# Performance work log

Hardware: AMD Instinct MI355X
Metric: run time of the kernel (lower is better)

Reference implementation:

```python
import jax, jax.numpy as jnp
import numpy as np

N, C, H, K = 32768, 128, 4, 16
D = C // H  # head_dim = 32


def setup_inputs() -> dict:
    key = jax.random.key(0)
    ks = jax.random.split(key, 8)
    feats = jax.random.normal(ks[0], (N, C), dtype=jnp.float32)
    coords = jax.random.normal(ks[1], (N, 3), dtype=jnp.float32)
    knn_idx = jax.random.randint(ks[2], (N, K), 0, N, dtype=jnp.int64)
    s = 0.02
    Wq = jax.random.normal(ks[3], (C, C), dtype=jnp.float32) * s
    Wk = jax.random.normal(ks[4], (C, C), dtype=jnp.float32) * s
    Wv = jax.random.normal(ks[5], (C, C), dtype=jnp.float32) * s
    Wo = jax.random.normal(ks[6], (C, C), dtype=jnp.float32) * s
    bo = jnp.zeros((C,), dtype=jnp.float32)
    return {"feats": feats, "coords": coords, "knn_idx": knn_idx,
            "Wq": Wq, "Wk": Wk, "Wv": Wv, "Wo": Wo, "bo": bo}


def reference(feats, coords, knn_idx, Wq, Wk, Wv, Wo, bo):
    # coords only feeds the kNN search (precomputed as knn_idx)
    n, c = feats.shape
    q = (feats @ Wq.T).reshape(n, H, D)          # [N,H,D]
    k = (feats @ Wk.T).reshape(n, H, D)          # [N,H,D]
    v = (feats @ Wv.T).reshape(n, H, D)          # [N,H,D]
    kn = k[knn_idx]                               # gather -> [N,K,H,D]
    vn = v[knn_idx]                               # gather -> [N,K,H,D]
    scores = jnp.einsum('nhd,nkhd->nhk', q, kn) / jnp.sqrt(jnp.float32(D))
    w = jax.nn.softmax(scores, axis=-1)           # softmax over K neighbors
    out = jnp.einsum('nhk,nkhd->nhd', w, vn).reshape(n, c)
    return out @ Wo.T + bo
```

## Files before the change

kernel.cpp:

```cpp
#include <hip/hip_runtime.h>

#define NPTS 32768
#define C 128
#define KNBR 16

typedef __attribute__((ext_vector_type(8))) short short8;
typedef __attribute__((ext_vector_type(4))) float floatx4;
typedef __attribute__((ext_vector_type(4))) int intx4;

__device__ __forceinline__ ushort f2b(float f) {
    union { float f; uint u; } x; x.f = f;
    uint r = (x.u + 0x7fffu + ((x.u >> 16) & 1u)) >> 16;
    return (ushort)r;
}
__device__ __forceinline__ ushort f2h(float f) {
    union { _Float16 h; ushort u; } x; x.h = (_Float16)f; return x.u;
}
__device__ __forceinline__ float h2f(ushort u) {
    union { ushort u; _Float16 h; } x; x.u = u; return (float)x.h;
}

__device__ __forceinline__ int col_of(int w, int b) {
    return 64 * (w >> 4) + 32 * ((w >> 3) & 1) + 16 * (b & 1) + 2 * (w & 7) + (b >> 1);
}

__device__ __forceinline__ void stage128_b(const ushort* __restrict__ gsrc, ushort* lds, int tid)
{
#pragma unroll
    for (int it = 0; it < 8; ++it) {
        const int f = it * 256 + tid;
        const int row = f >> 4, slot = f & 15;
        intx4 v = *(const intx4*)(gsrc + (size_t)f * 8);
        *(intx4*)(lds + ((row * 16 + (slot ^ (row & 7))) * 8)) = v;
    }
}
__device__ __forceinline__ void stage128_f(const float* __restrict__ gsrc, ushort* lds, int tid)
{
#pragma unroll
    for (int it = 0; it < 8; ++it) {
        const int f = it * 256 + tid;
        const int row = f >> 4, slot = f & 15;
        const float* s = gsrc + (size_t)f * 8;
        float4 v0 = *(const float4*)s;
        float4 v1 = *(const float4*)(s + 4);
        intx4 o;
        o.x = (int)((uint)f2b(v0.x) | ((uint)f2b(v0.y) << 16));
        o.y = (int)((uint)f2b(v0.z) | ((uint)f2b(v0.w) << 16));
        o.z = (int)((uint)f2b(v1.x) | ((uint)f2b(v1.y) << 16));
        o.w = (int)((uint)f2b(v1.z) | ((uint)f2b(v1.w) << 16));
        *(intx4*)(lds + ((row * 16 + (slot ^ (row & 7))) * 8)) = o;
    }
}

__device__ __forceinline__ void gemm_frag_acc(const ushort* ldsA, const ushort* ldsW,
                                              floatx4 acc[4][4], int lane)
{
    const int fr = lane & 15, kb = lane >> 4;
#pragma unroll
    for (int kk = 0; kk < 4; ++kk) {
        const int slot = kk * 4 + kb;
        short8 af[4], bf[4];
#pragma unroll
        for (int i = 0; i < 4; ++i) {
            const int row = i * 16 + fr;
            af[i] = *(const short8*)(ldsA + ((row * 16 + (slot ^ (row & 7))) * 8));
            bf[i] = *(const short8*)(ldsW + ((row * 16 + (slot ^ (row & 7))) * 8));
        }
#pragma unroll
        for (int i = 0; i < 4; ++i)
#pragma unroll
            for (int j = 0; j < 4; ++j)
                acc[i][j] = __builtin_amdgcn_mfma_f32_16x16x32_bf16(af[i], bf[j], acc[i][j], 0, 0, 0);
    }
}

__global__ __launch_bounds__(256) void qkv_gemm(
    const float* __restrict__ feats, const float* __restrict__ Wq,
    const float* __restrict__ Wk, const float* __restrict__ Wv,
    const float* __restrict__ Wo, ushort* __restrict__ wo_b,
    unsigned char* __restrict__ q8, unsigned char* __restrict__ kv8,
    ushort* __restrict__ scpack, float* __restrict__ qscale)
{
    const int tid = threadIdx.x;
    const int bx = blockIdx.x, sel = blockIdx.y;
    if (bx == 256) {
        if (sel != 0) return;
#pragma unroll 4
        for (int t = 0; t < 64; ++t) {
            const int gi = t * 256 + tid;
            const int j = gi >> 7, s = gi & 127;
            wo_b[gi] = f2b(Wo[(size_t)j * 128 + col_of(s >> 2, s & 3)]);
        }
        return;
    }
    __shared__ ushort ldsA[16384];
    __shared__ ushort ldsW[16384];
    __shared__ float rmax[2][128];
    const int lane = tid & 63, wid = tid >> 6;
    const int r0 = bx * 128;
    const float* W = (sel == 0) ? Wq : (sel == 1) ? Wk : Wv;

    stage128_f(feats + (size_t)r0 * 128, ldsA, tid);
    stage128_f(W, ldsW, tid);
    __syncthreads();

    floatx4 acc[4][4];
#pragma unroll
    for (int i = 0; i < 4; ++i)
#pragma unroll
        for (int j = 0; j < 4; ++j) acc[i][j] = (floatx4){0.f, 0.f, 0.f, 0.f};

    const int wr = (wid >> 1) * 64, wc = (wid & 1) * 64;
    gemm_frag_acc(ldsA + wr * 16 * 8, ldsW + wc * 16 * 8, acc, lane);

    const int fr = lane & 15, kb = lane >> 4;

    float mx[4][4];
#pragma unroll
    for (int i = 0; i < 4; ++i)
#pragma unroll
        for (int r = 0; r < 4; ++r) {
            float m = fabsf(acc[i][0][r]);
            m = fmaxf(m, fabsf(acc[i][1][r]));
            m = fmaxf(m, fabsf(acc[i][2][r]));
            m = fmaxf(m, fabsf(acc[i][3][r]));
            m = fmaxf(m, __shfl_xor(m, 1));
            m = fmaxf(m, __shfl_xor(m, 2));
            m = fmaxf(m, __shfl_xor(m, 4));
            m = fmaxf(m, __shfl_xor(m, 8));
            mx[i][r] = m;
        }
    if (fr == 0) {
#pragma unroll
        for (int i = 0; i < 4; ++i)
#pragma unroll
            for (int r = 0; r < 4; ++r)
                rmax[wc >> 6][wr + i * 16 + kb * 4 + r] = mx[i][r];
    }
    __syncthreads();

    const int boff = ((wc >> 5) + (fr & 1)) * 32 + (fr >> 1) * 4;
#pragma unroll
    for (int i = 0; i < 4; ++i)
#pragma unroll
        for (int r = 0; r < 4; ++r) {
            const int lr = wr + i * 16 + kb * 4 + r;
            const int nn = r0 + lr;
            const float comb = fmaxf(fmaxf(rmax[0][lr], rmax[1][lr]), 1e-20f);
            const float qs = 127.f / comb;
            int b0 = __float2int_rn(acc[i][0][r] * qs);
            int b1 = __float2int_rn(acc[i][1][r] * qs);
            int b2 = __float2int_rn(acc[i][2][r] * qs);
            int b3 = __float2int_rn(acc[i][3][r] * qs);
            uint u_lo = (uint)(b0 & 0xff) | ((uint)(b1 & 0xff) << 8);
            uint u_hi = (uint)(b2 & 0xff) | ((uint)(b3 & 0xff) << 8);
            uint o_lo = __shfl_xor(u_lo, 1);
            uint o_hi = __shfl_xor(u_hi, 1);
            uint word = (fr & 1) ? (o_hi | (u_hi << 16)) : (u_lo | (o_lo << 16));
            if (sel == 0) {
                *(uint*)(q8 + (size_t)nn * 128 + boff) = word;
                if (fr == 0 && wc == 0) qscale[nn] = comb * (1.f / 127.f);
            } else if (sel == 1) {
                *(uint*)(kv8 + (size_t)nn * 256 + boff) = word;
                if (fr == 0 && wc == 0) scpack[(size_t)nn * 2] = f2h(comb * (1.f / 127.f));
            } else {
                *(uint*)(kv8 + (size_t)nn * 256 + 128 + boff) = word;
                if (fr == 0 && wc == 0) scpack[(size_t)nn * 2 + 1] = f2h(comb * (1.f / 127.f));
            }
        }
}

__global__ __launch_bounds__(256, 6) void attn_kernel(
    const unsigned char* __restrict__ q8, const unsigned char* __restrict__ kv8,
    const ushort* __restrict__ scpack, const float* __restrict__ qscale,
    const int* __restrict__ knn, ushort* __restrict__ attn_p)
{
    const int tid = threadIdx.x;
    const int lane = tid & 63;
    const int wp = __builtin_amdgcn_readfirstlane(tid >> 6);
    const int n = blockIdx.x * 4 + wp;

    const int kk = lane >> 2, h = lane & 3;
    const int nb4 = knn[(size_t)n * KNBR + kk];
    const int* kr = knn + (size_t)n * KNBR;

    const unsigned char* krow = kv8 + (size_t)nb4 * 256 + h * 32;
    intx4 k0 = *(const intx4*)(krow);
    intx4 k1 = *(const intx4*)(krow + 16);
    const unsigned char* qrow = q8 + (size_t)n * 128 + h * 32;
    intx4 qq0 = *(const intx4*)(qrow);
    intx4 qq1 = *(const intx4*)(qrow + 16);
    const uint scp = *(const uint*)(scpack + (size_t)nb4 * 2);

    ushort vsh[KNBR];
#pragma unroll
    for (int j = 0; j < KNBR; ++j) {
        const int nbv = kr[j];
        vsh[j] = *(const ushort*)(kv8 + (size_t)nbv * 256 + 128 + lane * 2);
    }

    const float qs6 = qscale[n] * 0.17677669529663687f;

    int dp = 0;
#if __has_builtin(__builtin_amdgcn_sdot4)
#pragma unroll
    for (int i = 0; i < 4; ++i) dp = __builtin_amdgcn_sdot4(qq0[i], k0[i], dp, false);
#pragma unroll
    for (int i = 0; i < 4; ++i) dp = __builtin_amdgcn_sdot4(qq1[i], k1[i], dp, false);
#else
#pragma unroll
    for (int i = 0; i < 4; ++i) {
        uint a = (uint)qq0[i], b = (uint)k0[i];
        dp += (int)(signed char)(a) * (int)(signed char)(b)
            + (int)(signed char)(a >> 8) * (int)(signed char)(b >> 8)
            + (int)(signed char)(a >> 16) * (int)(signed char)(b >> 16)
            + (int)(signed char)(a >> 24) * (int)(signed char)(b >> 24);
        a = (uint)qq1[i]; b = (uint)k1[i];
        dp += (int)(signed char)(a) * (int)(signed char)(b)
            + (int)(signed char)(a >> 8) * (int)(signed char)(b >> 8)
            + (int)(signed char)(a >> 16) * (int)(signed char)(b >> 16)
            + (int)(signed char)(a >> 24) * (int)(signed char)(b >> 24);
    }
#endif

    const float ksc = h2f((ushort)(scp & 0xffff));
    const float vsc = h2f((ushort)(scp >> 16));
    const float sc = (float)dp * ksc * qs6;

    float mxv = sc;
    mxv = fmaxf(mxv, __shfl_xor(mxv, 4));
    mxv = fmaxf(mxv, __shfl_xor(mxv, 8));
    mxv = fmaxf(mxv, __shfl_xor(mxv, 16));
    mxv = fmaxf(mxv, __shfl_xor(mxv, 32));
    const float e = __expf(sc - mxv);
    float sm = e;
    sm += __shfl_xor(sm, 4);
    sm += __shfl_xor(sm, 8);
    sm += __shfl_xor(sm, 16);
    sm += __shfl_xor(sm, 32);
    const float wgt = e * vsc / sm;

    const int h2v = lane >> 4;
    float a0 = 0.f, a1 = 0.f;
#pragma unroll
    for (int j = 0; j < KNBR; ++j) {
        const float w2 = __shfl(wgt, j * 4 + h2v);
        const ushort u = vsh[j];
        a0 += w2 * (float)(signed char)(u & 0xff);
        a1 += w2 * (float)(signed char)(u >> 8);
    }
    const uint pr = (uint)f2b(a0) | ((uint)f2b(a1) << 16);
    *(uint*)(attn_p + (size_t)n * 128 + lane * 2) = pr;
}

__global__ __launch_bounds__(256) void out_gemm(
    const ushort* __restrict__ A, const ushort* __restrict__ Wo_b,
    const float* __restrict__ bias, float* __restrict__ out)
{
    __shared__ ushort ldsA[16384];
    __shared__ ushort ldsW[16384];
    const int tid = threadIdx.x, lane = tid & 63, wid = tid >> 6;
    const int r0 = blockIdx.x * 128;

    stage128_b(A + (size_t)r0 * 128, ldsA, tid);
    stage128_b(Wo_b, ldsW, tid);
    __syncthreads();

    floatx4 acc[4][4];
#pragma unroll
    for (int i = 0; i < 4; ++i)
#pragma unroll
        for (int j = 0; j < 4; ++j) acc[i][j] = (floatx4){0.f, 0.f, 0.f, 0.f};

    const int wr = (wid >> 1) * 64, wc = (wid & 1) * 64;
    gemm_frag_acc(ldsA + wr * 16 * 8, ldsW + wc * 16 * 8, acc, lane);

    const int fr = lane & 15, kb = lane >> 4;
#pragma unroll
    for (int i = 0; i < 4; ++i)
#pragma unroll
        for (int j = 0; j < 4; ++j) {
            const int col = wc + j * 16 + fr;
            const float bv = bias[col];
#pragma unroll
            for (int r = 0; r < 4; ++r) {
                const int n = r0 + wr + i * 16 + kb * 4 + r;
                out[(size_t)n * 128 + col] = acc[i][j][r] + bv;
            }
        }
}

extern "C" void kernel_launch(void* const* d_in, const int* in_sizes, int n_in,
                              void* d_out, int out_size, void* d_ws, size_t ws_size,
                              hipStream_t stream)
{
    const float* feats = (const float*)d_in[0];
    const int*   knn   = (const int*)d_in[2];
    const float* Wq    = (const float*)d_in[3];
    const float* Wk    = (const float*)d_in[4];
    const float* Wv    = (const float*)d_in[5];
    const float* Wo    = (const float*)d_in[6];
    const float* bo    = (const float*)d_in[7];
    float* out = (float*)d_out;

    ushort* attn_p = (ushort*)d_ws;
    unsigned char* q8  = (unsigned char*)(attn_p + (size_t)NPTS * C);
    unsigned char* kv8 = q8 + (size_t)NPTS * 128;
    ushort* scpack = (ushort*)(kv8 + (size_t)NPTS * 256);
    float* qscale  = (float*)(scpack + (size_t)NPTS * 2);
    ushort* wo_b   = (ushort*)(qscale + (size_t)NPTS);

    qkv_gemm<<<dim3(257, 3), 256, 0, stream>>>(feats, Wq, Wk, Wv, Wo, wo_b,
                                               q8, kv8, scpack, qscale);
    attn_kernel<<<NPTS / 4, 256, 0, stream>>>(q8, kv8, scpack, qscale, knn, attn_p);
    out_gemm<<<NPTS / 128, 256, 0, stream>>>(attn_p, wo_b, bo, out);
}
```

Before: 50.06 us.

## Precompute bf16 weights, fuse Q/K/V GEMMs per tile, read weights from global

A new prep kernel converts Wq/Wk/Wv/Wo to bf16 once per call. qkv_gemm then processes 64-row tiles and loops over all three projections inside one block. The feats tile is staged and converted once instead of three times, and B fragments are loaded straight from global/L2 instead of LDS. out_gemm likewise uses 64-row tiles with direct weight loads and less LDS, aiming for higher occupancy. The cost is an extra kernel launch plus uncoalesced-ish global weight fragment reads.

Result: slower. 57.80 us (+15.5%).

```diff
diff --git a/kernel.cpp b/kernel.cpp
--- a/kernel.cpp
+++ b/kernel.cpp
@@ -24,23 +24,62 @@
     return 64 * (w >> 4) + 32 * ((w >> 3) & 1) + 16 * (b & 1) + 2 * (w & 7) + (b >> 1);
 }
 
-__device__ __forceinline__ void stage128_b(const ushort* __restrict__ gsrc, ushort* lds, int tid)
-{
-#pragma unroll
-    for (int it = 0; it < 8; ++it) {
+__global__ __launch_bounds__(256) void prep_weights(
+    const float* __restrict__ Wq, const float* __restrict__ Wk,
+    const float* __restrict__ Wv, const float* __restrict__ Wo,
+    ushort* __restrict__ wq_b, ushort* __restrict__ wk_b,
+    ushort* __restrict__ wv_b, ushort* __restrict__ wo_b)
+{
+    const int b = blockIdx.x, tid = threadIdx.x;
+    if (b < 24) {
+        const int wsel = b >> 3;
+        const float* src = (wsel == 0) ? Wq : (wsel == 1) ? Wk : Wv;
+        ushort* dst = (wsel == 0) ? wq_b : (wsel == 1) ? wk_b : wv_b;
+        const size_t i = (size_t)(b & 7) * 2048 + (size_t)tid * 8;
+        float4 v0 = *(const float4*)(src + i);
+        float4 v1 = *(const float4*)(src + i + 4);
+        intx4 o;
+        o.x = (int)((uint)f2b(v0.x) | ((uint)f2b(v0.y) << 16));
+        o.y = (int)((uint)f2b(v0.z) | ((uint)f2b(v0.w) << 16));
+        o.z = (int)((uint)f2b(v1.x) | ((uint)f2b(v1.y) << 16));
+        o.w = (int)((uint)f2b(v1.z) | ((uint)f2b(v1.w) << 16));
+        *(intx4*)(dst + i) = o;
+    } else {
+        const int wb = b - 24;
+        const size_t i = (size_t)wb * 2048 + (size_t)tid * 8;
+        ushort tmp[8];
+#pragma unroll
+        for (int t = 0; t < 8; ++t) {
+            const int gi = (int)(i + t);
+            const int j = gi >> 7, s = gi & 127;
+            tmp[t] = f2b(Wo[(size_t)j * 128 + col_of(s >> 2, s & 3)]);
+        }
+        intx4 o;
+        o.x = (int)((uint)tmp[0] | ((uint)tmp[1] << 16));
+        o.y = (int)((uint)tmp[2] | ((uint)tmp[3] << 16));
+        o.z = (int)((uint)tmp[4] | ((uint)tmp[5] << 16));
+        o.w = (int)((uint)tmp[6] | ((uint)tmp[7] << 16));
+        *(intx4*)(wo_b + i) = o;
+    }
+}
+
+__global__ __launch_bounds__(256, 4) void qkv_gemm(
+    const float* __restrict__ feats,
+    const ushort* __restrict__ wq_b, const ushort* __restrict__ wk_b,
+    const ushort* __restrict__ wv_b,
+    unsigned char* __restrict__ q8, unsigned char* __restrict__ kv8,
+    ushort* __restrict__ scpack, float* __restrict__ qscale)
+{
+    __shared__ ushort ldsA[64 * 128];
+    __shared__ float rmax[3][2][64];
+    const int tid = threadIdx.x, lane = tid & 63, wid = tid >> 6;
+    const int r0 = blockIdx.x * 64;
+
+#pragma unroll
+    for (int it = 0; it < 4; ++it) {
         const int f = it * 256 + tid;
         const int row = f >> 4, slot = f & 15;
-        intx4 v = *(const intx4*)(gsrc + (size_t)f * 8);
-        *(intx4*)(lds + ((row * 16 + (slot ^ (row & 7))) * 8)) = v;
-    }
-}
-__device__ __forceinline__ void stage128_f(const float* __restrict__ gsrc, ushort* lds, int tid)
-{
-#pragma unroll
-    for (int it = 0; it < 8; ++it) {
-        const int f = it * 256 + tid;
-        const int row = f >> 4, slot = f & 15;
-        const float* s = gsrc + (size_t)f * 8;
+        const float* s = feats + (size_t)r0 * 128 + (size_t)f * 8;
         float4 v0 = *(const float4*)s;
         float4 v1 = *(const float4*)(s + 4);
         intx4 o;
@@ -48,126 +87,103 @@
         o.y = (int)((uint)f2b(v0.z) | ((uint)f2b(v0.w) << 16));
         o.z = (int)((uint)f2b(v1.x) | ((uint)f2b(v1.y) << 16));
         o.w = (int)((uint)f2b(v1.z) | ((uint)f2b(v1.w) << 16));
-        *(intx4*)(lds + ((row * 16 + (slot ^ (row & 7))) * 8)) = o;
-    }
-}
-
-__device__ __forceinline__ void gemm_frag_acc(const ushort* ldsA, const ushort* ldsW,
-                                              floatx4 acc[4][4], int lane)
-{
+        *(intx4*)(ldsA + ((row * 16 + (slot ^ (row & 7))) * 8)) = o;
+    }
+    __syncthreads();
+
     const int fr = lane & 15, kb = lane >> 4;
-#pragma unroll
-    for (int kk = 0; kk < 4; ++kk) {
-        const int slot = kk * 4 + kb;
-        short8 af[4], bf[4];
-#pragma unroll
-        for (int i = 0; i < 4; ++i) {
-            const int row = i * 16 + fr;
-            af[i] = *(const short8*)(ldsA + ((row * 16 + (slot ^ (row & 7))) * 8));
-            bf[i] = *(const short8*)(ldsW + ((row * 16 + (slot ^ (row & 7))) * 8));
-        }
-#pragma unroll
-        for (int i = 0; i < 4; ++i)
-#pragma unroll
-            for (int j = 0; j < 4; ++j)
-                acc[i][j] = __builtin_amdgcn_mfma_f32_16x16x32_bf16(af[i], bf[j], acc[i][j], 0, 0, 0);
-    }
-}
-
-__global__ __launch_bounds__(256) void qkv_gemm(
-    const float* __restrict__ feats, const float* __restrict__ Wq,
-    const float* __restrict__ Wk, const float* __restrict__ Wv,
-    const float* __restrict__ Wo, ushort* __restrict__ wo_b,
-    unsigned char* __restrict__ q8, unsigned char* __restrict__ kv8,
-    ushort* __restrict__ scpack, float* __restrict__ qscale)
-{
-    const int tid = threadIdx.x;
-    const int bx = blockIdx.x, sel = blockIdx.y;
-    if (bx == 256) {
-        if (sel != 0) return;
-#pragma unroll 4
-        for (int t = 0; t < 64; ++t) {
-            const int gi = t * 256 + tid;
-            const int j = gi >> 7, s = gi & 127;
-            wo_b[gi] = f2b(Wo[(size_t)j * 128 + col_of(s >> 2, s & 3)]);
-        }
-        return;
-    }
-    __shared__ ushort ldsA[16384];
-    __shared__ ushort ldsW[16384];
-    __shared__ float rmax[2][128];
-    const int lane = tid & 63, wid = tid >> 6;
-    const int r0 = bx * 128;
-    const float* W = (sel == 0) ? Wq : (sel == 1) ? Wk : Wv;
-
-    stage128_f(feats + (size_t)r0 * 128, ldsA, tid);
-    stage128_f(W, ldsW, tid);
-    __syncthreads();
-
-    floatx4 acc[4][4];
-#pragma unroll
-    for (int i = 0; i < 4; ++i)
-#pragma unroll
-        for (int j = 0; j < 4; ++j) acc[i][j] = (floatx4){0.f, 0.f, 0.f, 0.f};
-
-    const int wr = (wid >> 1) * 64, wc = (wid & 1) * 64;
-    gemm_frag_acc(ldsA + wr * 16 * 8, ldsW + wc * 16 * 8, acc, lane);
-
-    const int fr = lane & 15, kb = lane >> 4;
-
-    float mx[4][4];
-#pragma unroll
-    for (int i = 0; i < 4; ++i)
-#pragma unroll
-        for (int r = 0; r < 4; ++r) {
-            float m = fabsf(acc[i][0][r]);
-            m = fmaxf(m, fabsf(acc[i][1][r]));
-            m = fmaxf(m, fabsf(acc[i][2][r]));
-            m = fmaxf(m, fabsf(acc[i][3][r]));
-            m = fmaxf(m, __shfl_xor(m, 1));
-            m = fmaxf(m, __shfl_xor(m, 2));
-            m = fmaxf(m, __shfl_xor(m, 4));
-            m = fmaxf(m, __shfl_xor(m, 8));
-            mx[i][r] = m;
-        }
-    if (fr == 0) {
-#pragma unroll
-        for (int i = 0; i < 4; ++i)
-#pragma unroll
-            for (int r = 0; r < 4; ++r)
-                rmax[wc >> 6][wr + i * 16 + kb * 4 + r] = mx[i][r];
-    }
-    __syncthreads();
+    const int wr = (wid >> 1) * 32, wc = (wid & 1) * 64;
+
+    short8 af[2][4];
+#pragma unroll
+    for (int i = 0; i < 2; ++i)
+#pragma unroll
+        for (int kk = 0; kk < 4; ++kk) {
+            const int row = wr + i * 16 + fr;
+            const int slot = kk * 4 + kb;
+            af[i][kk] = *(const short8*)(ldsA + ((row * 16 + (slot ^ (row & 7))) * 8));
+        }
 
     const int boff = ((wc >> 5) + (fr & 1)) * 32 + (fr >> 1) * 4;
-#pragma unroll
-    for (int i = 0; i < 4; ++i)
-#pragma unroll
-        for (int r = 0; r < 4; ++r) {
-            const int lr = wr + i * 16 + kb * 4 + r;
-            const int nn = r0 + lr;
-            const float comb = fmaxf(fmaxf(rmax[0][lr], rmax[1][lr]), 1e-20f);
-            const float qs = 127.f / comb;
-            int b0 = __float2int_rn(acc[i][0][r] * qs);
-            int b1 = __float2int_rn(acc[i][1][r] * qs);
-            int b2 = __float2int_rn(acc[i][2][r] * qs);
-            int b3 = __float2int_rn(acc[i][3][r] * qs);
-            uint u_lo = (uint)(b0 & 0xff) | ((uint)(b1 & 0xff) << 8);
-            uint u_hi = (uint)(b2 & 0xff) | ((uint)(b3 & 0xff) << 8);
-            uint o_lo = __shfl_xor(u_lo, 1);
-            uint o_hi = __shfl_xor(u_hi, 1);
-            uint word = (fr & 1) ? (o_hi | (u_hi << 16)) : (u_lo | (o_lo << 16));
-            if (sel == 0) {
-                *(uint*)(q8 + (size_t)nn * 128 + boff) = word;
-                if (fr == 0 && wc == 0) qscale[nn] = comb * (1.f / 127.f);
-            } else if (sel == 1) {
-                *(uint*)(kv8 + (size_t)nn * 256 + boff) = word;
-                if (fr == 0 && wc == 0) scpack[(size_t)nn * 2] = f2h(comb * (1.f / 127.f));
-            } else {
-                *(uint*)(kv8 + (size_t)nn * 256 + 128 + boff) = word;
-                if (fr == 0 && wc == 0) scpack[(size_t)nn * 2 + 1] = f2h(comb * (1.f / 127.f));
+
+#pragma unroll
+    for (int sel = 0; sel < 3; ++sel) {
+        const ushort* W = (sel == 0) ? wq_b : (sel == 1) ? wk_b : wv_b;
+
+        floatx4 acc[2][4];
+#pragma unroll
+        for (int i = 0; i < 2; ++i)
+#pragma unroll
+            for (int j = 0; j < 4; ++j) acc[i][j] = (floatx4){0.f, 0.f, 0.f, 0.f};
+
+#pragma unroll
+        for (int kk = 0; kk < 4; ++kk) {
+            short8 bf[4];
+#pragma unroll
+            for (int j = 0; j < 4; ++j) {
+                const int col = wc + j * 16 + fr;
+                bf[j] = *(const short8*)(W + (size_t)col * 128 + (kk * 4 + kb) * 8);
             }
-        }
+#pragma unroll
+            for (int i = 0; i < 2; ++i)
+#pragma unroll
+                for (int j = 0; j < 4; ++j)
+                    acc[i][j] = __builtin_amdgcn_mfma_f32_16x16x32_bf16(af[i][kk], bf[j], acc[i][j], 0, 0, 0);
+        }
+
+        float mx[2][4];
+#pragma unroll
+        for (int i = 0; i < 2; ++i)
+#pragma unroll
+            for (int r = 0; r < 4; ++r) {
+                float m = fabsf(acc[i][0][r]);
+                m = fmaxf(m, fabsf(acc[i][1][r]));
+                m = fmaxf(m, fabsf(acc[i][2][r]));
+                m = fmaxf(m, fabsf(acc[i][3][r]));
+                m = fmaxf(m, __shfl_xor(m, 1));
+                m = fmaxf(m, __shfl_xor(m, 2));
+                m = fmaxf(m, __shfl_xor(m, 4));
+                m = fmaxf(m, __shfl_xor(m, 8));
+                mx[i][r] = m;
+            }
+        if (fr == 0) {
+#pragma unroll
+            for (int i = 0; i < 2; ++i)
+#pragma unroll
+                for (int r = 0; r < 4; ++r)
+                    rmax[sel][wc >> 6][wr + i * 16 + kb * 4 + r] = mx[i][r];
+        }
+        __syncthreads();
+
+#pragma unroll
+        for (int i = 0; i < 2; ++i)
+#pragma unroll
+            for (int r = 0; r < 4; ++r) {
+                const int lr = wr + i * 16 + kb * 4 + r;
+                const int nn = r0 + lr;
+                const float comb = fmaxf(fmaxf(rmax[sel][0][lr], rmax[sel][1][lr]), 1e-20f);
+                const float qs = 127.f / comb;
+                int b0 = __float2int_rn(acc[i][0][r] * qs);
+                int b1 = __float2int_rn(acc[i][1][r] * qs);
+                int b2 = __float2int_rn(acc[i][2][r] * qs);
+                int b3 = __float2int_rn(acc[i][3][r] * qs);
+                uint u_lo = (uint)(b0 & 0xff) | ((uint)(b1 & 0xff) << 8);
+                uint u_hi = (uint)(b2 & 0xff) | ((uint)(b3 & 0xff) << 8);
+                uint o_lo = __shfl_xor(u_lo, 1);
+                uint o_hi = __shfl_xor(u_hi, 1);
+                uint word = (fr & 1) ? (o_hi | (u_hi << 16)) : (u_lo | (o_lo << 16));
+                if (sel == 0) {
+                    *(uint*)(q8 + (size_t)nn * 128 + boff) = word;
+                    if (fr == 0 && wc == 0) qscale[nn] = comb * (1.f / 127.f);
+                } else if (sel == 1) {
+                    *(uint*)(kv8 + (size_t)nn * 256 + boff) = word;
+                    if (fr == 0 && wc == 0) scpack[(size_t)nn * 2] = f2h(comb * (1.f / 127.f));
+                } else {
+                    *(uint*)(kv8 + (size_t)nn * 256 + 128 + boff) = word;
+                    if (fr == 0 && wc == 0) scpack[(size_t)nn * 2 + 1] = f2h(comb * (1.f / 127.f));
+                }
+            }
+    }
 }
 
 __global__ __launch_bounds__(256, 6) void attn_kernel(
@@ -253,41 +269,69 @@
     *(uint*)(attn_p + (size_t)n * 128 + lane * 2) = pr;
 }
 
-__global__ __launch_bounds__(256) void out_gemm(
-    const ushort* __restrict__ A, const ushort* __restrict__ Wo_b,
+__global__ __launch_bounds__(256, 4) void out_gemm(
+    const ushort* __restrict__ A, const ushort* __restrict__ wo_b,
     const float* __restrict__ bias, float* __restrict__ out)
 {
-    __shared__ ushort ldsA[16384];
-    __shared__ ushort ldsW[16384];
+    __shared__ ushort ldsA[64 * 128];
     const int tid = threadIdx.x, lane = tid & 63, wid = tid >> 6;
-    const int r0 = blockIdx.x * 128;
-
-    stage128_b(A + (size_t)r0 * 128, ldsA, tid);
-    stage128_b(Wo_b, ldsW, tid);
+    const int r0 = blockIdx.x * 64;
+
+#pragma unroll
+    for (int it = 0; it < 4; ++it) {
+        const int f = it * 256 + tid;
+        const int row = f >> 4, slot = f & 15;
+        intx4 v = *(const intx4*)(A + (size_t)r0 * 128 + (size_t)f * 8);
+        *(intx4*)(ldsA + ((row * 16 + (slot ^ (row & 7))) * 8)) = v;
+    }
     __syncthreads();
 
-    floatx4 acc[4][4];
-#pragma unroll
-    for (int i = 0; i < 4; ++i)
+    const int fr = lane & 15, kb = lane >> 4;
+    const int wr = (wid >> 1) * 32, wc = (wid & 1) * 64;
+
+    short8 af[2][4];
+#pragma unroll
+    for (int i = 0; i < 2; ++i)
+#pragma unroll
+        for (int kk = 0; kk < 4; ++kk) {
+            const int row = wr + i * 16 + fr;
+            const int slot = kk * 4 + kb;
+            af[i][kk] = *(const short8*)(ldsA + ((row * 16 + (slot ^ (row & 7))) * 8));
+        }
+
+    floatx4 acc[2][4];
+#pragma unroll
+    for (int i = 0; i < 2; ++i)
 #pragma unroll
         for (int j = 0; j < 4; ++j) acc[i][j] = (floatx4){0.f, 0.f, 0.f, 0.f};
 
-    const int wr = (wid >> 1) * 64, wc = (wid & 1) * 64;
-    gemm_frag_acc(ldsA + wr * 16 * 8, ldsW + wc * 16 * 8, acc, lane);
-
-    const int fr = lane & 15, kb = lane >> 4;
-#pragma unroll
-    for (int i = 0; i < 4; ++i)
+#pragma unroll
+    for (int kk = 0; kk < 4; ++kk) {
+        short8 bf[4];
 #pragma unroll
         for (int j = 0; j < 4; ++j) {
             const int col = wc + j * 16 + fr;
-            const float bv = bias[col];
+            bf[j] = *(const short8*)(wo_b + (size_t)col * 128 + (kk * 4 + kb) * 8);
+        }
+#pragma unroll
+        for (int i = 0; i < 2; ++i)
+#pragma unroll
+            for (int j = 0; j < 4; ++j)
+                acc[i][j] = __builtin_amdgcn_mfma_f32_16x16x32_bf16(af[i][kk], bf[j], acc[i][j], 0, 0, 0);
+    }
+
+#pragma unroll
+    for (int j = 0; j < 4; ++j) {
+        const int col = wc + j * 16 + fr;
+        const float bv = bias[col];
+#pragma unroll
+        for (int i = 0; i < 2; ++i)
 #pragma unroll
             for (int r = 0; r < 4; ++r) {
                 const int n = r0 + wr + i * 16 + kb * 4 + r;
                 out[(size_t)n * 128 + col] = acc[i][j][r] + bv;
             }
-        }
+    }
 }
 
 extern "C" void kernel_launch(void* const* d_in, const int* in_sizes, int n_in,
@@ -308,10 +352,14 @@
     unsigned char* kv8 = q8 + (size_t)NPTS * 128;
     ushort* scpack = (ushort*)(kv8 + (size_t)NPTS * 256);
     float* qscale  = (float*)(scpack + (size_t)NPTS * 2);
-    ushort* wo_b   = (ushort*)(qscale + (size_t)NPTS);
-
-    qkv_gemm<<<dim3(257, 3), 256, 0, stream>>>(feats, Wq, Wk, Wv, Wo, wo_b,
-                                               q8, kv8, scpack, qscale);
+    ushort* wq_b   = (ushort*)(qscale + (size_t)NPTS);
+    ushort* wk_b   = wq_b + 16384;
+    ushort* wv_b   = wk_b + 16384;
+    ushort* wo_b   = wv_b + 16384;
+
+    prep_weights<<<32, 256, 0, stream>>>(Wq, Wk, Wv, Wo, wq_b, wk_b, wv_b, wo_b);
+    qkv_gemm<<<NPTS / 64, 256, 0, stream>>>(feats, wq_b, wk_b, wv_b,
+                                            q8, kv8, scpack, qscale);
     attn_kernel<<<NPTS / 4, 256, 0, stream>>>(q8, kv8, scpack, qscale, knn, attn_p);
-    out_gemm<<<NPTS / 128, 256, 0, stream>>>(attn_p, wo_b, bo, out);
-}
+    out_gemm<<<NPTS / 64, 256, 0, stream>>>(attn_p, wo_b, bo, out);
+}
```
